# Optimization experiments

Hardware: AMD Instinct MI355X
Metric: run time of the kernel (lower is better)

## Reference

```python
import jax, jax.numpy as jnp
import numpy as np

N, F, H, E, R = 100000, 256, 64, 800000, 7
EPS = 1e-5

def _layernorm(x, g, b):
    mu = jnp.mean(x, axis=-1, keepdims=True)
    var = jnp.mean((x - mu) ** 2, axis=-1, keepdims=True)
    return (x - mu) * jax.lax.rsqrt(var + EPS) * g + b

def setup_inputs() -> dict:
    key = jax.random.key(0)
    ks = jax.random.split(key, 16)
    block_features = jax.random.normal(ks[0], (N, F), dtype=jnp.float32)
    src = jax.random.randint(ks[1], (E,), 0, N).astype(jnp.float32)
    dst = jax.random.randint(ks[2], (E,), 0, N).astype(jnp.float32)
    rel = jax.random.randint(ks[3], (E,), 0, R).astype(jnp.float32)
    w = jax.random.uniform(ks[4], (E,), dtype=jnp.float32)
    typed_edges = jnp.stack([src, dst, rel, w], axis=1)  # [E,4]
    def lin(k, fan_in, fan_out):
        s = 1.0 / np.sqrt(fan_in)
        k1, k2 = jax.random.split(k)
        return (jax.random.uniform(k1, (fan_in, fan_out), jnp.float32, -s, s),
                jax.random.uniform(k2, (fan_out,), jnp.float32, -s, s))
    W1, b1 = lin(ks[5], F, H)
    W2, b2 = lin(ks[6], H, H)
    rel_emb = jax.random.normal(ks[7], (R, H), dtype=jnp.float32)
    Wm1, bm1 = lin(ks[8], 3 * H + 1, H)
    Wm2, bm2 = lin(ks[9], H, H)
    Wg1, bg1 = lin(ks[10], 2 * H, H)
    Wg2, bg2 = lin(ks[11], H, H)
    return dict(block_features=block_features, typed_edges=typed_edges,
                W1=W1, b1=b1, g1=jnp.ones(H), be1=jnp.zeros(H), W2=W2, b2=b2,
                rel_emb=rel_emb, Wm1=Wm1, bm1=bm1, Wm2=Wm2, bm2=bm2,
                gn=jnp.ones(H), bn=jnp.zeros(H), Wg1=Wg1, bg1=bg1, Wg2=Wg2, bg2=bg2)

def reference(block_features, typed_edges, W1, b1, g1, be1, W2, b2, rel_emb,
              Wm1, bm1, Wm2, bm2, gn, bn, Wg1, bg1, Wg2, bg2):
    # node_proj: Linear -> LN -> ReLU -> Linear -> ReLU
    h = jax.nn.relu(_layernorm(block_features @ W1 + b1, g1, be1))
    h = jax.nn.relu(h @ W2 + b2)  # [N,H]
    src = typed_edges[:, 0].astype(jnp.int32)
    dst = typed_edges[:, 1].astype(jnp.int32)
    rel = typed_edges[:, 2].astype(jnp.int32)
    w = typed_edges[:, 3:4]  # [E,1]
    m_in = jnp.concatenate([h[src], h[dst], rel_emb[rel], w], axis=-1)  # [E,3H+1]
    msg = jax.nn.relu(m_in @ Wm1 + bm1) @ Wm2 + bm2  # [E,H]
    agg = jax.ops.segment_sum(msg, dst, num_segments=h.shape[0])  # [N,H]
    nodes = _layernorm(h + agg, gn, bn)
    g = jnp.concatenate([nodes.mean(axis=0), nodes.max(axis=0)], axis=-1)  # [2H]
    return jax.nn.relu(g @ Wg1 + bg1) @ Wg2 + bg2  # [H]
```

## Files before the change

kernel.cpp:

```cpp
#include <hip/hip_runtime.h>

typedef unsigned short u16;
typedef unsigned int   u32;
typedef __attribute__((ext_vector_type(8))) short bf16x8;
typedef __attribute__((ext_vector_type(4))) float f32x4;

#define EPS 1e-5f
#define MFMA(a,b,c) __builtin_amdgcn_mfma_f32_16x16x32_bf16(a,b,c,0,0,0)

constexpr int OB_b1=0, OB_g1=64, OB_be1=128, OB_b2=192, OB_bm1=256, OB_w192=320,
              OB_bm2=384, OB_gn=448, OB_bn=512, OB_bg1=576, OB_bg2=640,
              OB_Wg1=704, OB_Wg2=8896, WB_TOT=12992;
constexpr int FR_Wm1=0;
constexpr int FR_Wm2=12288;
constexpr int FR_rel=16384;
constexpr int FR_W1 =16960;
constexpr int FR_W2 =33344;
constexpr int FR_TOT=37440;

__device__ __forceinline__ float bf2f(u32 u) { return __uint_as_float(u << 16); }
__device__ __forceinline__ u16 f2bf(float f) {
  u32 b = __float_as_uint(f);
  return (u16)((b + 0x7fffu + ((b >> 16) & 1u)) >> 16);
}
__device__ __forceinline__ u32 fkey(float f) {
  u32 b = __float_as_uint(f);
  return (b & 0x80000000u) ? ~b : (b | 0x80000000u);
}

__launch_bounds__(256)
__global__ void k_prep(const float* __restrict__ W1, const float* __restrict__ b1,
                       const float* __restrict__ g1, const float* __restrict__ be1,
                       const float* __restrict__ W2, const float* __restrict__ b2,
                       const float* __restrict__ rel_emb,
                       const float* __restrict__ Wm1, const float* __restrict__ bm1,
                       const float* __restrict__ Wm2, const float* __restrict__ bm2,
                       const float* __restrict__ gn, const float* __restrict__ bn,
                       const float* __restrict__ Wg1, const float* __restrict__ bg1,
                       const float* __restrict__ Wg2, const float* __restrict__ bg2,
                       float* __restrict__ wbuf, u16* __restrict__ frags) {
  int tid = blockIdx.x * 256 + threadIdx.x;
  int nth = gridDim.x * 256;
  for (int i = tid; i < 64; i += nth) {
    wbuf[OB_b1 + i] = b1[i];   wbuf[OB_g1 + i] = g1[i];
    wbuf[OB_be1 + i] = be1[i]; wbuf[OB_b2 + i] = b2[i];
    wbuf[OB_bm1 + i] = bm1[i]; wbuf[OB_w192 + i] = Wm1[192 * 64 + i];
    wbuf[OB_bm2 + i] = bm2[i]; wbuf[OB_gn + i] = gn[i];
    wbuf[OB_bn + i] = bn[i];   wbuf[OB_bg1 + i] = bg1[i];
    wbuf[OB_bg2 + i] = bg2[i];
  }
  for (int i = tid; i < 8192; i += nth) wbuf[OB_Wg1 + i] = Wg1[i];
  for (int i = tid; i < 4096; i += nth) wbuf[OB_Wg2 + i] = Wg2[i];
  for (int idx = tid; idx < 16384; idx += nth) {
    int f = idx >> 9, L = (idx >> 3) & 63, j = idx & 7;
    int k = (f >> 2) * 32 + ((L >> 4) << 3) + j, n = ((f & 3) << 4) + (L & 15);
    frags[FR_W1 + idx] = f2bf(W1[k * 64 + n]);
  }
  for (int idx = tid; idx < 4096; idx += nth) {
    int f = idx >> 9, L = (idx >> 3) & 63, j = idx & 7;
    int k = (f >> 2) * 32 + ((L >> 4) << 3) + j, n = ((f & 3) << 4) + (L & 15);
    frags[FR_W2 + idx] = f2bf(W2[k * 64 + n]);
  }
  for (int idx = tid; idx < 12288; idx += nth) {
    int f = idx >> 9, L = (idx >> 3) & 63, j = idx & 7;
    int k = (f >> 2) * 32 + ((L >> 4) << 3) + j, n = ((f & 3) << 4) + (L & 15);
    frags[FR_Wm1 + idx] = f2bf(Wm1[k * 64 + n]);
  }
  for (int idx = tid; idx < 4096; idx += nth) {
    int f = idx >> 9, L = (idx >> 3) & 63, j = idx & 7;
    int k = (f >> 2) * 32 + ((L >> 4) << 3) + j, n = ((f & 3) << 4) + (L & 15);
    frags[FR_Wm2 + idx] = f2bf(Wm2[k * 64 + n]);
  }
  for (int idx = tid; idx < 576; idx += nth) {
    int r = idx / 80, c = idx % 80;
    frags[FR_rel + idx] = (r < 7 && c < 64) ? f2bf(rel_emb[r * 64 + c]) : (u16)0;
  }
}

__launch_bounds__(256, 3)
__global__ void k_h(const float* __restrict__ X, const float* __restrict__ wbuf,
                    const u16* __restrict__ frags, u16* __restrict__ hb, int N) {
  __shared__ __align__(16) u16 sW1[32 * 512];
  __shared__ __align__(16) u16 sW2[8 * 512];
  __shared__ __align__(16) u16 st[4][16 * 72];

  {
    const uint4* srcp = (const uint4*)(frags + FR_W1);
    uint4* d1 = (uint4*)sW1;
    for (int i = threadIdx.x; i < 2048; i += 256) d1[i] = srcp[i];
    const uint4* srcp2 = (const uint4*)(frags + FR_W2);
    uint4* d2 = (uint4*)sW2;
    for (int i = threadIdx.x; i < 512; i += 256) d2[i] = srcp2[i];
  }
  __syncthreads();

  int lane = threadIdx.x & 63, wave = threadIdx.x >> 6;
  int m = lane & 15, quad = lane >> 4, koff = quad * 8, col0 = m;

  float b1v[4], g1v[4], be1v[4], b2v[4];
  #pragma unroll
  for (int nt = 0; nt < 4; nt++) {
    int c = nt * 16 + col0;
    b1v[nt] = wbuf[OB_b1 + c]; g1v[nt] = wbuf[OB_g1 + c];
    be1v[nt] = wbuf[OB_be1 + c]; b2v[nt] = wbuf[OB_b2 + c];
  }

  int ntiles = (N + 15) / 16;
  int wid = blockIdx.x * 4 + wave, nw = gridDim.x * 4;
  for (int tile = wid; tile < ntiles; tile += nw) {
    int n0 = tile * 16;
    int nm = min(n0 + m, N - 1);
    const float* xr = X + (size_t)nm * 256 + koff;

    f32x4 acc[4] = {};
    #pragma unroll 1
    for (int ks = 0; ks < 8; ks++) {
      float4 u0 = *(const float4*)(xr + ks * 32);
      float4 u1 = *(const float4*)(xr + ks * 32 + 4);
      bf16x8 a;
      a[0] = (short)f2bf(u0.x); a[1] = (short)f2bf(u0.y);
      a[2] = (short)f2bf(u0.z); a[3] = (short)f2bf(u0.w);
      a[4] = (short)f2bf(u1.x); a[5] = (short)f2bf(u1.y);
      a[6] = (short)f2bf(u1.z); a[7] = (short)f2bf(u1.w);
      #pragma unroll
      for (int nt = 0; nt < 4; nt++) {
        bf16x8 b = *(const bf16x8*)(sW1 + (ks * 4 + nt) * 512 + lane * 8);
        acc[nt] = MFMA(a, b, acc[nt]);
      }
    }

    float v[4][4];
    #pragma unroll
    for (int nt = 0; nt < 4; nt++)
      #pragma unroll
      for (int r = 0; r < 4; r++) v[nt][r] = acc[nt][r] + b1v[nt];

    #pragma unroll
    for (int r = 0; r < 4; r++) {
      float s = v[0][r] + v[1][r] + v[2][r] + v[3][r];
      #pragma unroll
      for (int mk = 8; mk >= 1; mk >>= 1) s += __shfl_xor(s, mk, 64);
      float mu = s * (1.f / 64.f);
      float q = 0.f;
      #pragma unroll
      for (int nt = 0; nt < 4; nt++) { float d = v[nt][r] - mu; q += d * d; }
      #pragma unroll
      for (int mk = 8; mk >= 1; mk >>= 1) q += __shfl_xor(q, mk, 64);
      float rs = rsqrtf(q * (1.f / 64.f) + EPS);
      #pragma unroll
      for (int nt = 0; nt < 4; nt++) {
        float h1 = fmaxf(fmaf((v[nt][r] - mu) * rs, g1v[nt], be1v[nt]), 0.f);
        st[wave][(quad * 4 + r) * 72 + nt * 16 + col0] = f2bf(h1);
      }
    }
    __builtin_amdgcn_wave_barrier();

    f32x4 acc2[4] = {};
    #pragma unroll
    for (int ks = 0; ks < 2; ks++) {
      bf16x8 a2 = *(const bf16x8*)(st[wave] + m * 72 + ks * 32 + koff);
      #pragma unroll
      for (int nt = 0; nt < 4; nt++) {
        bf16x8 b = *(const bf16x8*)(sW2 + (ks * 4 + nt) * 512 + lane * 8);
        acc2[nt] = MFMA(a2, b, acc2[nt]);
      }
    }
    __builtin_amdgcn_wave_barrier();

    #pragma unroll
    for (int nt = 0; nt < 4; nt++)
      #pragma unroll
      for (int r = 0; r < 4; r++) {
        int row = n0 + quad * 4 + r;
        if (row < N)
          hb[(size_t)row * 64 + nt * 16 + col0] = f2bf(fmaxf(acc2[nt][r] + b2v[nt], 0.f));
      }
  }
}

__launch_bounds__(256, 3)
__global__ void k_edge(const float* __restrict__ te, const u16* __restrict__ hb,
                       const float* __restrict__ wbuf, const u16* __restrict__ frags,
                       float* __restrict__ agg, int E, int N) {
  __shared__ __align__(16) u16 sWm1[24 * 512];
  __shared__ __align__(16) u16 sWm2[8 * 512];
  __shared__ __align__(16) u16 srel[576];
  __shared__ __align__(16) u16 st[4][16 * 72];

  {
    const uint4* s1 = (const uint4*)(frags + FR_Wm1);
    uint4* d1 = (uint4*)sWm1;
    for (int i = threadIdx.x; i < 1536; i += 256) d1[i] = s1[i];
    const uint4* s2 = (const uint4*)(frags + FR_Wm2);
    uint4* d2 = (uint4*)sWm2;
    for (int i = threadIdx.x; i < 512; i += 256) d2[i] = s2[i];
    const uint4* s3 = (const uint4*)(frags + FR_rel);
    uint4* d3 = (uint4*)srel;
    for (int i = threadIdx.x; i < 72; i += 256) d3[i] = s3[i];
  }
  __syncthreads();

  int lane = threadIdx.x & 63, wave = threadIdx.x >> 6;
  int m = lane & 15, quad = lane >> 4, koff = quad * 8, col0 = m;

  float bm1v[4], w192v[4], bm2v[4];
  #pragma unroll
  for (int nt = 0; nt < 4; nt++) {
    int c = nt * 16 + col0;
    bm1v[nt] = wbuf[OB_bm1 + c];
    w192v[nt] = wbuf[OB_w192 + c];
    bm2v[nt] = wbuf[OB_bm2 + c];
  }

  int ntiles = (E + 15) / 16;
  int wid = blockIdx.x * 4 + wave, nw = gridDim.x * 4;
  for (int tile = wid; tile < ntiles; tile += nw) {
    int e0 = tile * 16;
    int src = 0, dst = 0, rel = 0; float w = 0.f;
    if (lane < 16) {
      int e = min(e0 + lane, E - 1);
      float4 v = *(const float4*)(te + (size_t)e * 4);
      src = min(max((int)v.x, 0), N - 1);
      dst = min(max((int)v.y, 0), N - 1);
      rel = min(max((int)v.z, 0), 6);
      w = v.w;
    }
    int src_m = __shfl(src, m, 64);
    int dst_m = __shfl(dst, m, 64);
    int rel_m = __shfl(rel, m, 64);

    const u16* hs = hb + (size_t)src_m * 64;
    const u16* hd = hb + (size_t)dst_m * 64;
    bf16x8 af[6];
    af[0] = *(const bf16x8*)(hs + koff);
    af[1] = *(const bf16x8*)(hs + 32 + koff);
    af[2] = *(const bf16x8*)(hd + koff);
    af[3] = *(const bf16x8*)(hd + 32 + koff);
    af[4] = *(const bf16x8*)(srel + rel_m * 80 + koff);
    af[5] = *(const bf16x8*)(srel + rel_m * 80 + 32 + koff);

    f32x4 acc[4] = {};
    #pragma unroll
    for (int ks = 0; ks < 6; ks++) {
      #pragma unroll
      for (int nt = 0; nt < 4; nt++) {
        bf16x8 b = *(const bf16x8*)(sWm1 + (ks * 4 + nt) * 512 + lane * 8);
        acc[nt] = MFMA(af[ks], b, acc[nt]);
      }
    }

    float wrow[4];
    #pragma unroll
    for (int r = 0; r < 4; r++) wrow[r] = __shfl(w, quad * 4 + r, 64);
    #pragma unroll
    for (int nt = 0; nt < 4; nt++)
      #pragma unroll
      for (int r = 0; r < 4; r++) {
        float v = fmaf(wrow[r], w192v[nt], acc[nt][r] + bm1v[nt]);
        st[wave][(quad * 4 + r) * 72 + nt * 16 + col0] = f2bf(fmaxf(v, 0.f));
      }
    __builtin_amdgcn_wave_barrier();

    f32x4 acc2[4] = {};
    #pragma unroll
    for (int ks = 0; ks < 2; ks++) {
      bf16x8 a2 = *(const bf16x8*)(st[wave] + m * 72 + ks * 32 + koff);
      #pragma unroll
      for (int nt = 0; nt < 4; nt++) {
        bf16x8 b = *(const bf16x8*)(sWm2 + (ks * 4 + nt) * 512 + lane * 8);
        acc2[nt] = MFMA(a2, b, acc2[nt]);
      }
    }
    __builtin_amdgcn_wave_barrier();

    int dstr[4]; bool valr[4];
    #pragma unroll
    for (int r = 0; r < 4; r++) {
      int row = quad * 4 + r;
      dstr[r] = __shfl(dst, row, 64);
      valr[r] = (e0 + row) < E;
    }
    #pragma unroll
    for (int nt = 0; nt < 4; nt++)
      #pragma unroll
      for (int r = 0; r < 4; r++)
        if (valr[r])
          atomicAdd(agg + (size_t)dstr[r] * 64 + nt * 16 + col0, acc2[nt][r] + bm2v[nt]);
  }
}

__launch_bounds__(256)
__global__ void k_nodes(const u16* __restrict__ hb, const float* __restrict__ agg,
                        const float* __restrict__ wbuf, float* __restrict__ gsum,
                        u32* __restrict__ gmax, int N) {
  int lane = threadIdx.x & 63, wave = threadIdx.x >> 6;
  int wid = blockIdx.x * 4 + wave;
  int nw = gridDim.x * 4;
  float gn = wbuf[OB_gn + lane], bn = wbuf[OB_bn + lane];
  float sj = 0.f, mj = -3.0e38f;
  for (int n = wid; n < N; n += nw) {
    float v = bf2f(hb[(size_t)n * 64 + lane]) + agg[(size_t)n * 64 + lane];
    float s = v;
    #pragma unroll
    for (int m = 32; m >= 1; m >>= 1) s += __shfl_xor(s, m, 64);
    float mu = s * (1.f / 64.f);
    float d = v - mu;
    float q = d * d;
    #pragma unroll
    for (int m = 32; m >= 1; m >>= 1) q += __shfl_xor(q, m, 64);
    float rs = rsqrtf(q * (1.f / 64.f) + EPS);
    float val = fmaf(d * rs, gn, bn);
    sj += val;
    mj = fmaxf(mj, val);
  }
  __shared__ float bs[256], bm[256];
  bs[threadIdx.x] = sj;
  bm[threadIdx.x] = mj;
  __syncthreads();
  if (threadIdx.x < 64) {
    int t = threadIdx.x;
    float ts = bs[t] + bs[64 + t] + bs[128 + t] + bs[192 + t];
    float tm = fmaxf(fmaxf(bm[t], bm[64 + t]), fmaxf(bm[128 + t], bm[192 + t]));
    atomicAdd(gsum + t, ts);
    atomicMax(gmax + t, fkey(tm));
  }
}

__launch_bounds__(128)
__global__ void k_final(const float* __restrict__ wbuf, const float* __restrict__ gsum,
                        const u32* __restrict__ gmax, float* __restrict__ out, int N) {
  __shared__ float g[128];
  __shared__ float y1[64];
  int t = threadIdx.x;
  if (t < 64) {
    g[t] = gsum[t] / (float)N;
  } else {
    u32 k = gmax[t - 64];
    u32 b = (k & 0x80000000u) ? (k & 0x7fffffffu) : ~k;
    g[t] = __uint_as_float(b);
  }
  __syncthreads();
  if (t < 64) {
    float a = wbuf[OB_bg1 + t];
    for (int i = 0; i < 128; i++) a = fmaf(g[i], wbuf[OB_Wg1 + i * 64 + t], a);
    y1[t] = fmaxf(a, 0.f);
  }
  __syncthreads();
  if (t < 64) {
    float a = wbuf[OB_bg2 + t];
    for (int k = 0; k < 64; k++) a = fmaf(y1[k], wbuf[OB_Wg2 + k * 64 + t], a);
    out[t] = a;
  }
}

extern "C" void kernel_launch(void* const* d_in, const int* in_sizes, int n_in,
                              void* d_out, int out_size, void* d_ws, size_t ws_size,
                              hipStream_t stream) {
  const int N = in_sizes[0] / 256;
  const int E = in_sizes[1] / 4;

  char* ws = (char*)d_ws;
  size_t aggB = (size_t)N * 64 * 4;
  size_t hbB  = (size_t)N * 64 * 2;
  float* agg   = (float*)ws;
  u16*   hb    = (u16*)(ws + aggB);
  float* gsum  = (float*)(ws + aggB + hbB);
  u32*   gmax  = (u32*)(ws + aggB + hbB + 256);
  float* wbuf  = (float*)(ws + aggB + hbB + 512);
  u16*   frags = (u16*)(ws + aggB + hbB + 512 + (size_t)WB_TOT * 4);

  const float* X  = (const float*)d_in[0];
  const float* te = (const float*)d_in[1];

  hipLaunchKernelGGL(k_prep, dim3(64), dim3(256), 0, stream,
                     (const float*)d_in[2], (const float*)d_in[3], (const float*)d_in[4],
                     (const float*)d_in[5], (const float*)d_in[6], (const float*)d_in[7],
                     (const float*)d_in[8], (const float*)d_in[9], (const float*)d_in[10],
                     (const float*)d_in[11], (const float*)d_in[12], (const float*)d_in[13],
                     (const float*)d_in[14], (const float*)d_in[15], (const float*)d_in[16],
                     (const float*)d_in[17], (const float*)d_in[18], wbuf, frags);
  hipMemsetAsync(agg, 0, aggB, stream);
  hipMemsetAsync(gsum, 0, 512, stream);
  hipLaunchKernelGGL(k_h, dim3(640), dim3(256), 0, stream, X, wbuf, frags, hb, N);
  hipLaunchKernelGGL(k_edge, dim3(768), dim3(256), 0, stream, te, hb, wbuf, frags, agg, E, N);
  hipLaunchKernelGGL(k_nodes, dim3(2048), dim3(256), 0, stream, hb, agg, wbuf, gsum, gmax, N);
  hipLaunchKernelGGL(k_final, dim3(1), dim3(128), 0, stream, wbuf, gsum, gmax, (float*)d_out, N);
}
```

Baseline: 438.7 us.

## Software-pipeline edge gathers and double block size in edge kernel

The edge kernel now prefetches the next tile's edge record and gathered node-feature fragments while the current tile's first MFMA stage runs, so gather latency overlaps with compute. Blocks grow from 256 to 512 threads (8 waves) with per-wave staging buffers, and the grid stays at 768 blocks, which doubles the total number of waves. The loop is restructured so the prefetch happens after the first matmul and the current destination and weight are held in separate registers. The extra live registers for the prefetched fragments raise register pressure, and the launch bound of 512 threads with 6 blocks may limit allocation or force spills.

```diff
diff --git a/kernel.cpp b/kernel.cpp
--- a/kernel.cpp
+++ b/kernel.cpp
@@ -178,25 +178,25 @@
   }
 }
 
-__launch_bounds__(256, 3)
+__launch_bounds__(512, 6)
 __global__ void k_edge(const float* __restrict__ te, const u16* __restrict__ hb,
                        const float* __restrict__ wbuf, const u16* __restrict__ frags,
                        float* __restrict__ agg, int E, int N) {
   __shared__ __align__(16) u16 sWm1[24 * 512];
   __shared__ __align__(16) u16 sWm2[8 * 512];
   __shared__ __align__(16) u16 srel[576];
-  __shared__ __align__(16) u16 st[4][16 * 72];
+  __shared__ __align__(16) u16 st[8][16 * 72];
 
   {
     const uint4* s1 = (const uint4*)(frags + FR_Wm1);
     uint4* d1 = (uint4*)sWm1;
-    for (int i = threadIdx.x; i < 1536; i += 256) d1[i] = s1[i];
+    for (int i = threadIdx.x; i < 1536; i += 512) d1[i] = s1[i];
     const uint4* s2 = (const uint4*)(frags + FR_Wm2);
     uint4* d2 = (uint4*)sWm2;
-    for (int i = threadIdx.x; i < 512; i += 256) d2[i] = s2[i];
+    for (int i = threadIdx.x; i < 512; i += 512) d2[i] = s2[i];
     const uint4* s3 = (const uint4*)(frags + FR_rel);
     uint4* d3 = (uint4*)srel;
-    for (int i = threadIdx.x; i < 72; i += 256) d3[i] = s3[i];
+    for (int i = threadIdx.x; i < 72; i += 512) d3[i] = s3[i];
   }
   __syncthreads();
 
@@ -213,45 +213,70 @@
   }
 
   int ntiles = (E + 15) / 16;
-  int wid = blockIdx.x * 4 + wave, nw = gridDim.x * 4;
-  for (int tile = wid; tile < ntiles; tile += nw) {
-    int e0 = tile * 16;
-    int src = 0, dst = 0, rel = 0; float w = 0.f;
+  int wid = blockIdx.x * 8 + wave, nw = gridDim.x * 8;
+
+  int tile = wid;
+  int src = 0, dstv = 0, rel = 0; float w = 0.f;
+  bf16x8 af[6];
+
+  if (tile < ntiles) {
     if (lane < 16) {
-      int e = min(e0 + lane, E - 1);
+      int e = min(tile * 16 + lane, E - 1);
       float4 v = *(const float4*)(te + (size_t)e * 4);
-      src = min(max((int)v.x, 0), N - 1);
-      dst = min(max((int)v.y, 0), N - 1);
-      rel = min(max((int)v.z, 0), 6);
+      src  = min(max((int)v.x, 0), N - 1);
+      dstv = min(max((int)v.y, 0), N - 1);
+      rel  = min(max((int)v.z, 0), 6);
       w = v.w;
     }
-    int src_m = __shfl(src, m, 64);
-    int dst_m = __shfl(dst, m, 64);
-    int rel_m = __shfl(rel, m, 64);
-
-    const u16* hs = hb + (size_t)src_m * 64;
-    const u16* hd = hb + (size_t)dst_m * 64;
-    bf16x8 af[6];
+    int sm = __shfl(src, m, 64), dm = __shfl(dstv, m, 64), rm = __shfl(rel, m, 64);
+    const u16* hs = hb + (size_t)sm * 64;
+    const u16* hd = hb + (size_t)dm * 64;
     af[0] = *(const bf16x8*)(hs + koff);
     af[1] = *(const bf16x8*)(hs + 32 + koff);
     af[2] = *(const bf16x8*)(hd + koff);
     af[3] = *(const bf16x8*)(hd + 32 + koff);
-    af[4] = *(const bf16x8*)(srel + rel_m * 80 + koff);
-    af[5] = *(const bf16x8*)(srel + rel_m * 80 + 32 + koff);
+    af[4] = *(const bf16x8*)(srel + rm * 80 + koff);
+    af[5] = *(const bf16x8*)(srel + rm * 80 + 32 + koff);
+  }
+
+  while (tile < ntiles) {
+    int e0 = tile * 16;
+    int tile_n = tile + nw;
 
     f32x4 acc[4] = {};
     #pragma unroll
-    for (int ks = 0; ks < 6; ks++) {
+    for (int ks = 0; ks < 6; ks++)
       #pragma unroll
       for (int nt = 0; nt < 4; nt++) {
         bf16x8 b = *(const bf16x8*)(sWm1 + (ks * 4 + nt) * 512 + lane * 8);
         acc[nt] = MFMA(af[ks], b, acc[nt]);
       }
+
+    int dstc = dstv; float wc = w;
+
+    if (tile_n < ntiles) {
+      if (lane < 16) {
+        int e = min(tile_n * 16 + lane, E - 1);
+        float4 v = *(const float4*)(te + (size_t)e * 4);
+        src  = min(max((int)v.x, 0), N - 1);
+        dstv = min(max((int)v.y, 0), N - 1);
+        rel  = min(max((int)v.z, 0), 6);
+        w = v.w;
+      }
+      int sm = __shfl(src, m, 64), dm = __shfl(dstv, m, 64), rm = __shfl(rel, m, 64);
+      const u16* hs = hb + (size_t)sm * 64;
+      const u16* hd = hb + (size_t)dm * 64;
+      af[0] = *(const bf16x8*)(hs + koff);
+      af[1] = *(const bf16x8*)(hs + 32 + koff);
+      af[2] = *(const bf16x8*)(hd + koff);
+      af[3] = *(const bf16x8*)(hd + 32 + koff);
+      af[4] = *(const bf16x8*)(srel + rm * 80 + koff);
+      af[5] = *(const bf16x8*)(srel + rm * 80 + 32 + koff);
     }
 
     float wrow[4];
     #pragma unroll
-    for (int r = 0; r < 4; r++) wrow[r] = __shfl(w, quad * 4 + r, 64);
+    for (int r = 0; r < 4; r++) wrow[r] = __shfl(wc, quad * 4 + r, 64);
     #pragma unroll
     for (int nt = 0; nt < 4; nt++)
       #pragma unroll
@@ -273,19 +298,18 @@
     }
     __builtin_amdgcn_wave_barrier();
 
-    int dstr[4]; bool valr[4];
     #pragma unroll
     for (int r = 0; r < 4; r++) {
       int row = quad * 4 + r;
-      dstr[r] = __shfl(dst, row, 64);
-      valr[r] = (e0 + row) < E;
-    }
-    #pragma unroll
-    for (int nt = 0; nt < 4; nt++)
-      #pragma unroll
-      for (int r = 0; r < 4; r++)
-        if (valr[r])
-          atomicAdd(agg + (size_t)dstr[r] * 64 + nt * 16 + col0, acc2[nt][r] + bm2v[nt]);
+      int dr = __shfl(dstc, row, 64);
+      if (e0 + row < E) {
+        #pragma unroll
+        for (int nt = 0; nt < 4; nt++)
+          atomicAdd(agg + (size_t)dr * 64 + nt * 16 + col0, acc2[nt][r] + bm2v[nt]);
+      }
+    }
+
+    tile = tile_n;
   }
 }
 
@@ -382,7 +406,7 @@
   hipMemsetAsync(agg, 0, aggB, stream);
   hipMemsetAsync(gsum, 0, 512, stream);
   hipLaunchKernelGGL(k_h, dim3(640), dim3(256), 0, stream, X, wbuf, frags, hb, N);
-  hipLaunchKernelGGL(k_edge, dim3(768), dim3(256), 0, stream, te, hb, wbuf, frags, agg, E, N);
+  hipLaunchKernelGGL(k_edge, dim3(768), dim3(512), 0, stream, te, hb, wbuf, frags, agg, E, N);
   hipLaunchKernelGGL(k_nodes, dim3(2048), dim3(256), 0, stream, hb, agg, wbuf, gsum, gmax, N);
   hipLaunchKernelGGL(k_final, dim3(1), dim3(128), 0, stream, wbuf, gsum, gmax, (float*)d_out, N);
 }
```

Result: slower. 452.1 us (+3.1%).
